# Optimization experiments

Hardware: AMD Instinct MI355X
Metric: run time of the kernel (lower is better)

## Reference

```python
import jax, jax.numpy as jnp
import numpy as np

N = 10000      # num nodes
E = 320000     # num edges
IN = 256       # in_dim
MP = 256       # mp_width
FL = 512       # fl_width
OUT = 64       # out_dim


def setup_inputs() -> dict:
    key = jax.random.key(0)
    ks = jax.random.split(key, 20)
    inp = {}
    inp["x"] = jax.random.normal(ks[0], (N, IN), dtype=jnp.float32)
    inp["edge_index"] = jax.random.randint(ks[1], (2, E), 0, N, dtype=jnp.int64)
    # iMP (frozen) linear layers: weight ~ N(0, 1) per nn.init.normal_(std=1.0)
    inp["mp_w0"] = jax.random.normal(ks[2], (IN, MP), dtype=jnp.float32)
    inp["mp_b0"] = jax.random.uniform(ks[3], (MP,), minval=-1.0, maxval=1.0) / np.sqrt(IN)
    inp["mp_w1"] = jax.random.normal(ks[4], (MP, MP), dtype=jnp.float32)
    inp["mp_b1"] = jax.random.uniform(ks[5], (MP,), minval=-1.0, maxval=1.0) / np.sqrt(MP)
    inp["mp_w2"] = jax.random.normal(ks[6], (MP, MP), dtype=jnp.float32)
    inp["mp_b2"] = jax.random.uniform(ks[7], (MP,), minval=-1.0, maxval=1.0) / np.sqrt(MP)
    # FC layers (torch default Linear init scale ~ 1/sqrt(fan_in))
    inp["fc_w0"] = jax.random.normal(ks[8], (MP, FL), dtype=jnp.float32) / np.sqrt(MP)
    inp["fc_b0"] = jnp.zeros((FL,), dtype=jnp.float32)
    inp["fc_w1"] = jax.random.normal(ks[9], (FL, FL), dtype=jnp.float32) / np.sqrt(FL)
    inp["fc_b1"] = jnp.zeros((FL,), dtype=jnp.float32)
    # injection projections
    inp["inj_w0"] = jax.random.normal(ks[10], (MP, FL), dtype=jnp.float32) / np.sqrt(MP)
    inp["inj_b0"] = jnp.zeros((FL,), dtype=jnp.float32)
    inp["inj_w1"] = jax.random.normal(ks[11], (MP, FL), dtype=jnp.float32) / np.sqrt(MP)
    inp["inj_b1"] = jnp.zeros((FL,), dtype=jnp.float32)
    inp["alpha"] = jnp.array(1.0, dtype=jnp.float32)
    inp["out_w"] = jax.random.normal(ks[12], (FL, OUT), dtype=jnp.float32) / np.sqrt(FL)
    inp["out_b"] = jnp.zeros((OUT,), dtype=jnp.float32)
    return inp


def _imp(x, w, b, row, col, deg_inv):
    # h = relu(W x); h /= deg; Ah = scatter_add over row of h[col]
    h = jax.nn.relu(x @ w + b) * deg_inv[:, None]      # [N, out]
    return jnp.zeros_like(h).at[row].add(h[col])       # gather + scatter-add


def reference(x, edge_index, mp_w0, mp_b0, mp_w1, mp_b1, mp_w2, mp_b2,
              fc_w0, fc_b0, fc_w1, fc_b1, inj_w0, inj_b0, inj_w1, inj_b1,
              alpha, out_w, out_b):
    row, col = edge_index[0], edge_index[1]
    deg = jax.ops.segment_sum(jnp.ones((E,), x.dtype), col, num_segments=N)
    # nodes with deg==0 never appear in col so clamping does not change output
    deg_inv = 1.0 / jnp.maximum(deg, 1.0)

    h = _imp(x, mp_w0, mp_b0, row, col, deg_inv)
    h = _imp(h, mp_w1, mp_b1, row, col, deg_inv)
    h = _imp(h, mp_w2, mp_b2, row, col, deg_inv)

    x_inject = h
    h = alpha * (jax.nn.relu(h) @ fc_w0 + fc_b0) + (x_inject @ inj_w0 + inj_b0)
    h = alpha * (jax.nn.relu(h) @ fc_w1 + fc_b1) + (x_inject @ inj_w1 + inj_b1)
    return h @ out_w + out_b
```

## Files before the change

### kernel.cpp

```cpp
#include <hip/hip_runtime.h>

#define N_NODES 10000
#define N_EDGES 320000
#define MPAD 10112
#define NBIN 10048
#define CAP 128
#define EBLKS 157
#define PREP_BLOCKS 512
#define PREP_TOT 1148480L

typedef unsigned short u16;
typedef short bf16x8 __attribute__((ext_vector_type(8)));
typedef float f32x4 __attribute__((ext_vector_type(4)));

__device__ __forceinline__ u16 f2b(float f) {
  unsigned u = __builtin_bit_cast(unsigned, f);
  unsigned r = u + 0x7fffu + ((u >> 16) & 1u);
  return (u16)(r >> 16);
}
__device__ __forceinline__ unsigned pack2(float a, float b) {
  return (unsigned)f2b(a) | ((unsigned)f2b(b) << 16);
}
__device__ __forceinline__ float blo(unsigned u) { return __builtin_bit_cast(float, u << 16); }
__device__ __forceinline__ float bhi(unsigned u) { return __builtin_bit_cast(float, u & 0xffff0000u); }

struct PP {
  const float *x; const int *ei;
  const float *w0, *w1, *w2, *fcw0, *injw0, *fcw1, *injw1, *outw;
  const float *fcb0, *injb0, *fcb1, *injb1, *alpha, *outb;
  u16 *xb, *w0t, *w1t, *w2t, *wc1t, *wft;
  float *bias1, *bf;
  int *cursor, *deg; u16 *csr;
};

__global__ __launch_bounds__(256) void prep_place(PP P) {
  const int tid = threadIdx.x, bid = blockIdx.x;

  if (bid < EBLKS) {
    const int e0 = bid * 2048;
#pragma unroll
    for (int j = 0; j < 2048; j += 256) {
      int e = e0 + j + tid;
      if (e < N_EDGES) {
        int r = P.ei[e];
        int c = P.ei[N_EDGES + e];
        int pos = atomicAdd(&P.cursor[r], 1);
        if (pos < CAP) P.csr[r * CAP + pos] = (u16)c;
        atomicAdd(&P.deg[c], 1);
      }
    }
    return;
  }

  const float alpha = P.alpha[0];
  const long stride = (long)PREP_BLOCKS * 256;
  for (long ii = (long)(bid - EBLKS) * 256 + tid; ii < PREP_TOT; ii += stride) {
    long i = ii;
    if (i < 640000L) {
      float4 v = ((const float4*)P.x)[i];
      uint2 o;
      o.x = pack2(v.x, v.y);
      o.y = pack2(v.z, v.w);
      *(uint2*)(P.xb + 4 * i) = o;
      continue;
    }
    i -= 640000L;
    if (i < 65536) { P.w0t[i] = f2b(P.w0[(i & 255) * 256 + (i >> 8)]); continue; }
    i -= 65536;
    if (i < 65536) { P.w1t[i] = f2b(P.w1[(i & 255) * 256 + (i >> 8)]); continue; }
    i -= 65536;
    if (i < 65536) { P.w2t[i] = f2b(P.w2[(i & 255) * 256 + (i >> 8)]); continue; }
    i -= 65536;
    if (i < 262144) {
      int n = (int)(i >> 9), k = (int)(i & 511);
      float v = (k < 256) ? alpha * P.fcw0[k * 512 + n] : P.injw0[(k - 256) * 512 + n];
      P.wc1t[i] = f2b(v); continue;
    }
    i -= 262144;
    if (i < 49152) {
      int n = (int)(i & 63), k = (int)(i >> 6);
      const float* fr = (k < 512) ? P.fcw1 + (size_t)k * 512
                                  : P.injw1 + (size_t)(k - 512) * 512;
      float a0 = 0.f, a1 = 0.f, a2 = 0.f, a3 = 0.f;
#pragma unroll 4
      for (int j = 0; j < 512; j += 4) {
        float4 f = *(const float4*)(fr + j);
        a0 += f.x * P.outw[(j + 0) * 64 + n];
        a1 += f.y * P.outw[(j + 1) * 64 + n];
        a2 += f.z * P.outw[(j + 2) * 64 + n];
        a3 += f.w * P.outw[(j + 3) * 64 + n];
      }
      float acc = (a0 + a1) + (a2 + a3);
      if (k < 512) acc *= alpha;
      P.wft[n * 768 + k] = f2b(acc);
      continue;
    }
    i -= 49152;
    if (i < 64) {
      float acc = P.outb[i];
#pragma unroll 8
      for (int j = 0; j < 512; ++j)
        acc += (alpha * P.fcb1[j] + P.injb1[j]) * P.outw[j * 64 + i];
      P.bf[i] = acc;
      continue;
    }
    i -= 64;
    if (i < 512) { P.bias1[i] = alpha * P.fcb0[i] + P.injb0[i]; continue; }
  }
}

template<int K, bool RELU, bool SCALE, bool F32OUT>
__global__ __launch_bounds__(128) void gemm64(
    const u16* __restrict__ A, int lda,
    const u16* __restrict__ Bt,
    const float* __restrict__ bias,
    const int* __restrict__ deg,
    u16* __restrict__ Cb, float* __restrict__ Cf, int ldc)
{
  __shared__ u16 As[64 * 72];
  __shared__ u16 Bs[64 * 72];
  const int tid = threadIdx.x;
  const int m0 = blockIdx.x * 64;
  const int n0 = blockIdx.y * 64;
  const int wave = tid >> 6;
  const int lane = tid & 63;
  const int wr = wave * 32;
  const int lm = lane & 15;
  const int koff = (lane >> 4) * 8;

  const int srow = tid >> 2;
  const int scol = (tid & 3) * 16;
  const u16* Ag0 = A + (size_t)(m0 + srow) * lda + scol;
  const u16* Ag1 = A + (size_t)(m0 + srow + 32) * lda + scol;
  const u16* Bg0 = Bt + (size_t)(n0 + srow) * K + scol;
  const u16* Bg1 = Bt + (size_t)(n0 + srow + 32) * K + scol;
  u16* Asw0 = &As[srow * 72 + scol];
  u16* Asw1 = &As[(srow + 32) * 72 + scol];
  u16* Bsw0 = &Bs[srow * 72 + scol];
  u16* Bsw1 = &Bs[(srow + 32) * 72 + scol];

  f32x4 acc[2][4] = {};

  int4 pa0 = *(const int4*)(Ag0),     pa1 = *(const int4*)(Ag0 + 8);
  int4 pa2 = *(const int4*)(Ag1),     pa3 = *(const int4*)(Ag1 + 8);
  int4 pb0 = *(const int4*)(Bg0),     pb1 = *(const int4*)(Bg0 + 8);
  int4 pb2 = *(const int4*)(Bg1),     pb3 = *(const int4*)(Bg1 + 8);

#pragma unroll
  for (int kb = 0; kb < K; kb += 64) {
    __syncthreads();
    *(int4*)Asw0 = pa0; *(int4*)(Asw0 + 8) = pa1;
    *(int4*)Asw1 = pa2; *(int4*)(Asw1 + 8) = pa3;
    *(int4*)Bsw0 = pb0; *(int4*)(Bsw0 + 8) = pb1;
    *(int4*)Bsw1 = pb2; *(int4*)(Bsw1 + 8) = pb3;
    __syncthreads();
    if (kb + 64 < K) {
      pa0 = *(const int4*)(Ag0 + kb + 64); pa1 = *(const int4*)(Ag0 + kb + 72);
      pa2 = *(const int4*)(Ag1 + kb + 64); pa3 = *(const int4*)(Ag1 + kb + 72);
      pb0 = *(const int4*)(Bg0 + kb + 64); pb1 = *(const int4*)(Bg0 + kb + 72);
      pb2 = *(const int4*)(Bg1 + kb + 64); pb3 = *(const int4*)(Bg1 + kb + 72);
    }
#pragma unroll
    for (int ks = 0; ks < 2; ++ks) {
      bf16x8 af[2], bf[4];
#pragma unroll
      for (int mi = 0; mi < 2; ++mi)
        af[mi] = *(const bf16x8*)&As[(wr + mi * 16 + lm) * 72 + ks * 32 + koff];
#pragma unroll
      for (int ni = 0; ni < 4; ++ni)
        bf[ni] = *(const bf16x8*)&Bs[(ni * 16 + lm) * 72 + ks * 32 + koff];
#pragma unroll
      for (int mi = 0; mi < 2; ++mi)
#pragma unroll
        for (int ni = 0; ni < 4; ++ni)
          acc[mi][ni] = __builtin_amdgcn_mfma_f32_16x16x32_bf16(af[mi], bf[ni], acc[mi][ni], 0, 0, 0);
    }
  }

  const int q4 = (lane >> 4) * 4;
#pragma unroll
  for (int mi = 0; mi < 2; ++mi) {
#pragma unroll
    for (int ni = 0; ni < 4; ++ni) {
      const int gc = n0 + ni * 16 + lm;
      const float bv = bias[gc];
#pragma unroll
      for (int r = 0; r < 4; ++r) {
        const int gr = m0 + wr + mi * 16 + q4 + r;
        float v = acc[mi][ni][r] + bv;
        if (RELU) v = fmaxf(v, 0.f);
        if (SCALE) v *= 1.0f / fmaxf((float)deg[gr], 1.0f);
        if (F32OUT) {
          if (gr < N_NODES) Cf[(size_t)gr * ldc + gc] = v;
        } else {
          Cb[(size_t)gr * ldc + gc] = f2b(v);
        }
      }
    }
  }
}

__global__ __launch_bounds__(256) void gemm_fc1(
    const u16* __restrict__ A,
    const u16* __restrict__ Bt,
    const float* __restrict__ bias,
    u16* __restrict__ Cb)
{
  const int K = 512;
  __shared__ u16 As[64 * 72];
  __shared__ u16 Bs[128 * 72];
  const int tid = threadIdx.x;
  const int m0 = blockIdx.x * 64;
  const int n0 = blockIdx.y * 128;
  const int wave = tid >> 6;
  const int lane = tid & 63;
  const int wr = (wave >> 1) * 32;
  const int wc = (wave & 1) * 64;
  const int lm = lane & 15;
  const int koff = (lane >> 4) * 8;

  const int srow = tid >> 2;
  const int scol = (tid & 3) * 16;
  const u16* Ag  = A  + (size_t)(m0 + srow) * 512 + scol;
  const u16* Bg0 = Bt + (size_t)(n0 + srow) * K + scol;
  const u16* Bg1 = Bt + (size_t)(n0 + srow + 64) * K + scol;
  u16* Asw  = &As[srow * 72 + scol];
  u16* Bsw0 = &Bs[srow * 72 + scol];
  u16* Bsw1 = &Bs[(srow + 64) * 72 + scol];

  f32x4 acc[2][4] = {};

  int4 pa0 = *(const int4*)(Ag),      pa1 = *(const int4*)(Ag + 8);
  int4 pb0 = *(const int4*)(Bg0),     pb1 = *(const int4*)(Bg0 + 8);
  int4 pb2 = *(const int4*)(Bg1),     pb3 = *(const int4*)(Bg1 + 8);

#pragma unroll
  for (int kb = 0; kb < K; kb += 64) {
    __syncthreads();
    *(int4*)Asw = pa0;  *(int4*)(Asw + 8) = pa1;
    *(int4*)Bsw0 = pb0; *(int4*)(Bsw0 + 8) = pb1;
    *(int4*)Bsw1 = pb2; *(int4*)(Bsw1 + 8) = pb3;
    __syncthreads();
    if (kb + 64 < K) {
      pa0 = *(const int4*)(Ag + kb + 64);  pa1 = *(const int4*)(Ag + kb + 72);
      pb0 = *(const int4*)(Bg0 + kb + 64); pb1 = *(const int4*)(Bg0 + kb + 72);
      pb2 = *(const int4*)(Bg1 + kb + 64); pb3 = *(const int4*)(Bg1 + kb + 72);
    }
#pragma unroll
    for (int ks = 0; ks < 2; ++ks) {
      bf16x8 af[2], bf[4];
#pragma unroll
      for (int mi = 0; mi < 2; ++mi)
        af[mi] = *(const bf16x8*)&As[(wr + mi * 16 + lm) * 72 + ks * 32 + koff];
#pragma unroll
      for (int ni = 0; ni < 4; ++ni)
        bf[ni] = *(const bf16x8*)&Bs[(wc + ni * 16 + lm) * 72 + ks * 32 + koff];
#pragma unroll
      for (int mi = 0; mi < 2; ++mi)
#pragma unroll
        for (int ni = 0; ni < 4; ++ni)
          acc[mi][ni] = __builtin_amdgcn_mfma_f32_16x16x32_bf16(af[mi], bf[ni], acc[mi][ni], 0, 0, 0);
    }
  }

  const int q4 = (lane >> 4) * 4;
#pragma unroll
  for (int mi = 0; mi < 2; ++mi) {
#pragma unroll
    for (int ni = 0; ni < 4; ++ni) {
      const int gc = n0 + wc + ni * 16 + lm;
      const float bv = bias[gc];
#pragma unroll
      for (int r = 0; r < 4; ++r) {
        const int gr = m0 + wr + mi * 16 + q4 + r;
        Cb[(size_t)gr * 512 + gc] = f2b(fmaxf(acc[mi][ni][r] + bv, 0.f));
      }
    }
  }
}

__global__ __launch_bounds__(128) void gemm_fold(
    const u16* __restrict__ Ar,
    const u16* __restrict__ Ah,
    const u16* __restrict__ Bt,
    const float* __restrict__ bias,
    float* __restrict__ Cf)
{
  const int K = 768;
  __shared__ u16 As[64 * 72];
  __shared__ u16 Bs[64 * 72];
  const int tid = threadIdx.x;
  const int m0 = blockIdx.x * 64;
  const int n0 = 0;
  const int wave = tid >> 6;
  const int lane = tid & 63;
  const int wr = wave * 32;
  const int lm = lane & 15;
  const int koff = (lane >> 4) * 8;

  const int srow = tid >> 2;
  const int scol = (tid & 3) * 16;
  const int ar0 = m0 + srow, ar1 = m0 + srow + 32;
  auto aptr = [&](int row, int col) -> const u16* {
    return (col < 512) ? Ar + (size_t)row * 512 + col
                       : Ah + (size_t)row * 512 + (col - 512);
  };
  const u16* Bg0 = Bt + (size_t)(n0 + srow) * K + scol;
  const u16* Bg1 = Bt + (size_t)(n0 + srow + 32) * K + scol;
  u16* Asw0 = &As[srow * 72 + scol];
  u16* Asw1 = &As[(srow + 32) * 72 + scol];
  u16* Bsw0 = &Bs[srow * 72 + scol];
  u16* Bsw1 = &Bs[(srow + 32) * 72 + scol];

  f32x4 acc[2][4] = {};

  int4 pa0 = *(const int4*)aptr(ar0, scol);
  int4 pa1 = *(const int4*)aptr(ar0, scol + 8);
  int4 pa2 = *(const int4*)aptr(ar1, scol);
  int4 pa3 = *(const int4*)aptr(ar1, scol + 8);
  int4 pb0 = *(const int4*)(Bg0), pb1 = *(const int4*)(Bg0 + 8);
  int4 pb2 = *(const int4*)(Bg1), pb3 = *(const int4*)(Bg1 + 8);

#pragma unroll
  for (int kb = 0; kb < K; kb += 64) {
    __syncthreads();
    *(int4*)Asw0 = pa0; *(int4*)(Asw0 + 8) = pa1;
    *(int4*)Asw1 = pa2; *(int4*)(Asw1 + 8) = pa3;
    *(int4*)Bsw0 = pb0; *(int4*)(Bsw0 + 8) = pb1;
    *(int4*)Bsw1 = pb2; *(int4*)(Bsw1 + 8) = pb3;
    __syncthreads();
    if (kb + 64 < K) {
      int c = kb + 64 + scol;
      pa0 = *(const int4*)aptr(ar0, c);
      pa1 = *(const int4*)aptr(ar0, c + 8);
      pa2 = *(const int4*)aptr(ar1, c);
      pa3 = *(const int4*)aptr(ar1, c + 8);
      pb0 = *(const int4*)(Bg0 + kb + 64); pb1 = *(const int4*)(Bg0 + kb + 72);
      pb2 = *(const int4*)(Bg1 + kb + 64); pb3 = *(const int4*)(Bg1 + kb + 72);
    }
#pragma unroll
    for (int ks = 0; ks < 2; ++ks) {
      bf16x8 af[2], bf[4];
#pragma unroll
      for (int mi = 0; mi < 2; ++mi)
        af[mi] = *(const bf16x8*)&As[(wr + mi * 16 + lm) * 72 + ks * 32 + koff];
#pragma unroll
      for (int ni = 0; ni < 4; ++ni)
        bf[ni] = *(const bf16x8*)&Bs[(ni * 16 + lm) * 72 + ks * 32 + koff];
#pragma unroll
      for (int mi = 0; mi < 2; ++mi)
#pragma unroll
        for (int ni = 0; ni < 4; ++ni)
          acc[mi][ni] = __builtin_amdgcn_mfma_f32_16x16x32_bf16(af[mi], bf[ni], acc[mi][ni], 0, 0, 0);
    }
  }

  const int q4 = (lane >> 4) * 4;
#pragma unroll
  for (int mi = 0; mi < 2; ++mi) {
#pragma unroll
    for (int ni = 0; ni < 4; ++ni) {
      const int gc = ni * 16 + lm;
      const float bv = bias[gc];
#pragma unroll
      for (int r = 0; r < 4; ++r) {
        const int gr = m0 + wr + mi * 16 + q4 + r;
        if (gr < N_NODES) Cf[(size_t)gr * 64 + gc] = acc[mi][ni][r] + bv;
      }
    }
  }
}

__global__ __launch_bounds__(256) void aggregate(
    const u16* __restrict__ tmp, const int* __restrict__ cnt,
    const u16* __restrict__ csr, u16* __restrict__ out0,
    u16* __restrict__ A1, int mode)
{
  const int wv = threadIdx.x >> 6;
  const int lane = threadIdx.x & 63;
  const int r = blockIdx.x * 4 + wv;
  const int half = lane >> 5;
  const int q = lane & 31;
  int n = cnt[r]; if (n > CAP) n = CAP;
  const int beg = r * CAP, end = beg + n;
  const size_t feat = (size_t)q * 16;
  const char* tb = (const char*)tmp;

  float s0 = 0.f, s1 = 0.f, s2 = 0.f, s3 = 0.f, s4 = 0.f, s5 = 0.f, s6 = 0.f, s7 = 0.f;
  int i = beg;
  for (; i + 16 <= end; i += 16) {
    uint4 v[8];
#pragma unroll
    for (int j = 0; j < 8; ++j)
      v[j] = *(const uint4*)(tb + (size_t)csr[i + 2 * j + half] * 512 + feat);
#pragma unroll
    for (int j = 0; j < 8; ++j) {
      s0 += blo(v[j].x); s1 += bhi(v[j].x); s2 += blo(v[j].y); s3 += bhi(v[j].y);
      s4 += blo(v[j].z); s5 += bhi(v[j].z); s6 += blo(v[j].w); s7 += bhi(v[j].w);
    }
  }
  for (; i + 8 <= end; i += 8) {
    uint4 v[4];
#pragma unroll
    for (int j = 0; j < 4; ++j)
      v[j] = *(const uint4*)(tb + (size_t)csr[i + 2 * j + half] * 512 + feat);
#pragma unroll
    for (int j = 0; j < 4; ++j) {
      s0 += blo(v[j].x); s1 += bhi(v[j].x); s2 += blo(v[j].y); s3 += bhi(v[j].y);
      s4 += blo(v[j].z); s5 += bhi(v[j].z); s6 += blo(v[j].w); s7 += bhi(v[j].w);
    }
  }
  for (; i < end; i += 2) {
    int id = i + half;
    if (id < end) {
      uint4 v = *(const uint4*)(tb + (size_t)csr[id] * 512 + feat);
      s0 += blo(v.x); s1 += bhi(v.x); s2 += blo(v.y); s3 += bhi(v.y);
      s4 += blo(v.z); s5 += bhi(v.z); s6 += blo(v.w); s7 += bhi(v.w);
    }
  }
  const int src = lane ^ 32;
  s0 += __shfl(s0, src, 64); s1 += __shfl(s1, src, 64);
  s2 += __shfl(s2, src, 64); s3 += __shfl(s3, src, 64);
  s4 += __shfl(s4, src, 64); s5 += __shfl(s5, src, 64);
  s6 += __shfl(s6, src, 64); s7 += __shfl(s7, src, 64);

  if (half == 0) {
    uint4 pv;
    pv.x = pack2(s0, s1); pv.y = pack2(s2, s3);
    pv.z = pack2(s4, s5); pv.w = pack2(s6, s7);
    if (mode == 0) {
      *(uint4*)((char*)out0 + (size_t)r * 512 + feat) = pv;
    } else {
      uint4 pr;
      pr.x = pack2(fmaxf(s0, 0.f), fmaxf(s1, 0.f));
      pr.y = pack2(fmaxf(s2, 0.f), fmaxf(s3, 0.f));
      pr.z = pack2(fmaxf(s4, 0.f), fmaxf(s5, 0.f));
      pr.w = pack2(fmaxf(s6, 0.f), fmaxf(s7, 0.f));
      *(uint4*)((char*)A1 + (size_t)r * 1024 + feat) = pr;
      *(uint4*)((char*)A1 + (size_t)r * 1024 + 512 + feat) = pv;
    }
  }
}

extern "C" void kernel_launch(void* const* d_in, const int* in_sizes, int n_in,
                              void* d_out, int out_size, void* d_ws, size_t ws_size,
                              hipStream_t stream) {
  const int* ei = (const int*)d_in[1];

  char* p = (char*)d_ws;
  auto carve = [&](size_t bytes) -> void* {
    void* r = (void*)p;
    p += (bytes + 255) & ~(size_t)255;
    return r;
  };
  int*   deg     = (int*)carve(MPAD * 4);
  int*   cursor  = (int*)carve(NBIN * 4);
  u16*   csr     = (u16*)carve((size_t)NBIN * CAP * 2);
  float* bias1   = (float*)carve(512 * 4);
  float* bf      = (float*)carve(64 * 4);
  u16* xb    = (u16*)carve((size_t)MPAD * 256 * 2);
  u16* w0t   = (u16*)carve(65536 * 2);
  u16* w1t   = (u16*)carve(65536 * 2);
  u16* w2t   = (u16*)carve(65536 * 2);
  u16* wc1t  = (u16*)carve(262144 * 2);
  u16* wft   = (u16*)carve(49152 * 2);
  u16* tmp   = (u16*)carve((size_t)MPAD * 256 * 2);
  u16* h     = (u16*)carve((size_t)MPAD * 256 * 2);
  u16* cat1  = (u16*)carve((size_t)MPAD * 512 * 2);
  u16* relu1 = (u16*)carve((size_t)MPAD * 512 * 2);

  PP pp;
  pp.x = (const float*)d_in[0];
  pp.ei = ei;
  pp.w0 = (const float*)d_in[2];
  pp.w1 = (const float*)d_in[4];
  pp.w2 = (const float*)d_in[6];
  pp.fcw0 = (const float*)d_in[8];
  pp.fcw1 = (const float*)d_in[10];
  pp.injw0 = (const float*)d_in[12];
  pp.injw1 = (const float*)d_in[14];
  pp.outw = (const float*)d_in[17];
  pp.fcb0 = (const float*)d_in[9];
  pp.injb0 = (const float*)d_in[13];
  pp.fcb1 = (const float*)d_in[11];
  pp.injb1 = (const float*)d_in[15];
  pp.alpha = (const float*)d_in[16];
  pp.outb = (const float*)d_in[18];
  pp.xb = xb; pp.w0t = w0t; pp.w1t = w1t; pp.w2t = w2t;
  pp.wc1t = wc1t; pp.wft = wft;
  pp.bias1 = bias1; pp.bf = bf;
  pp.cursor = cursor; pp.deg = deg; pp.csr = csr;

  const float* mp_b0 = (const float*)d_in[3];
  const float* mp_b1 = (const float*)d_in[5];
  const float* mp_b2 = (const float*)d_in[7];
  float* out = (float*)d_out;

  hipMemsetAsync(deg, 0, (size_t)(MPAD + NBIN) * 4, stream);
  prep_place<<<EBLKS + PREP_BLOCKS, 256, 0, stream>>>(pp);

  dim3 gmp(MPAD / 64, 4), gfc(MPAD / 64, 4), go(MPAD / 64, 1);
  gemm64<256, true, true, false><<<gmp, 128, 0, stream>>>(xb, 256, w0t, mp_b0, deg, tmp, nullptr, 256);
  aggregate<<<2500, 256, 0, stream>>>(tmp, cursor, csr, h, nullptr, 0);
  gemm64<256, true, true, false><<<gmp, 128, 0, stream>>>(h, 256, w1t, mp_b1, deg, tmp, nullptr, 256);
  aggregate<<<2500, 256, 0, stream>>>(tmp, cursor, csr, h, nullptr, 0);
  gemm64<256, true, true, false><<<gmp, 128, 0, stream>>>(h, 256, w2t, mp_b2, deg, tmp, nullptr, 256);
  aggregate<<<2500, 256, 0, stream>>>(tmp, cursor, csr, nullptr, cat1, 1);
  gemm_fc1<<<gfc, 256, 0, stream>>>(cat1, wc1t, bias1, relu1);
  gemm_fold<<<go, 128, 0, stream>>>(relu1, cat1 + 256, wft, bf, out);
}
```

Measured before the change: 233.3 us.

## Use 4-wave blocks in MP GEMM and swap grid axes for A-tile reuse

The message-passing GEMM now uses 256-thread blocks with four waves, each owning 16 rows of the 64x64 tile instead of two waves owning 32 rows each. This halves the per-thread accumulators and global loads and raises waves per block. The grid axes are swapped in both the MP GEMM and the fc1 GEMM so that consecutive blocks share the same A row tile, which should improve L2 reuse of the activations. The unused F32OUT path is removed. Each wave now does less MFMA work per LDS read of B, so LDS traffic per flop goes up.

Measured after the change: 229.7 us. No clear change (-1.5%).

```diff
diff --git a/kernel.cpp b/kernel.cpp
--- a/kernel.cpp
+++ b/kernel.cpp
@@ -109,93 +109,72 @@
   }
 }
 
-template<int K, bool RELU, bool SCALE, bool F32OUT>
-__global__ __launch_bounds__(128) void gemm64(
+template<int K, bool RELU, bool SCALE>
+__global__ __launch_bounds__(256) void gemm64(
     const u16* __restrict__ A, int lda,
     const u16* __restrict__ Bt,
     const float* __restrict__ bias,
     const int* __restrict__ deg,
-    u16* __restrict__ Cb, float* __restrict__ Cf, int ldc)
+    u16* __restrict__ Cb, int ldc)
 {
   __shared__ u16 As[64 * 72];
   __shared__ u16 Bs[64 * 72];
   const int tid = threadIdx.x;
-  const int m0 = blockIdx.x * 64;
-  const int n0 = blockIdx.y * 64;
+  const int m0 = blockIdx.y * 64;
+  const int n0 = blockIdx.x * 64;
   const int wave = tid >> 6;
   const int lane = tid & 63;
-  const int wr = wave * 32;
+  const int wr = wave * 16;
   const int lm = lane & 15;
   const int koff = (lane >> 4) * 8;
 
   const int srow = tid >> 2;
   const int scol = (tid & 3) * 16;
-  const u16* Ag0 = A + (size_t)(m0 + srow) * lda + scol;
-  const u16* Ag1 = A + (size_t)(m0 + srow + 32) * lda + scol;
-  const u16* Bg0 = Bt + (size_t)(n0 + srow) * K + scol;
-  const u16* Bg1 = Bt + (size_t)(n0 + srow + 32) * K + scol;
-  u16* Asw0 = &As[srow * 72 + scol];
-  u16* Asw1 = &As[(srow + 32) * 72 + scol];
-  u16* Bsw0 = &Bs[srow * 72 + scol];
-  u16* Bsw1 = &Bs[(srow + 32) * 72 + scol];
-
-  f32x4 acc[2][4] = {};
-
-  int4 pa0 = *(const int4*)(Ag0),     pa1 = *(const int4*)(Ag0 + 8);
-  int4 pa2 = *(const int4*)(Ag1),     pa3 = *(const int4*)(Ag1 + 8);
-  int4 pb0 = *(const int4*)(Bg0),     pb1 = *(const int4*)(Bg0 + 8);
-  int4 pb2 = *(const int4*)(Bg1),     pb3 = *(const int4*)(Bg1 + 8);
+  const u16* Ag = A + (size_t)(m0 + srow) * lda + scol;
+  const u16* Bg = Bt + (size_t)(n0 + srow) * K + scol;
+  u16* Asw = &As[srow * 72 + scol];
+  u16* Bsw = &Bs[srow * 72 + scol];
+
+  f32x4 acc[4] = {};
+
+  int4 pa0 = *(const int4*)(Ag), pa1 = *(const int4*)(Ag + 8);
+  int4 pb0 = *(const int4*)(Bg), pb1 = *(const int4*)(Bg + 8);
 
 #pragma unroll
   for (int kb = 0; kb < K; kb += 64) {
     __syncthreads();
-    *(int4*)Asw0 = pa0; *(int4*)(Asw0 + 8) = pa1;
-    *(int4*)Asw1 = pa2; *(int4*)(Asw1 + 8) = pa3;
-    *(int4*)Bsw0 = pb0; *(int4*)(Bsw0 + 8) = pb1;
-    *(int4*)Bsw1 = pb2; *(int4*)(Bsw1 + 8) = pb3;
+    *(int4*)Asw = pa0; *(int4*)(Asw + 8) = pa1;
+    *(int4*)Bsw = pb0; *(int4*)(Bsw + 8) = pb1;
     __syncthreads();
     if (kb + 64 < K) {
-      pa0 = *(const int4*)(Ag0 + kb + 64); pa1 = *(const int4*)(Ag0 + kb + 72);
-      pa2 = *(const int4*)(Ag1 + kb + 64); pa3 = *(const int4*)(Ag1 + kb + 72);
-      pb0 = *(const int4*)(Bg0 + kb + 64); pb1 = *(const int4*)(Bg0 + kb + 72);
-      pb2 = *(const int4*)(Bg1 + kb + 64); pb3 = *(const int4*)(Bg1 + kb + 72);
+      pa0 = *(const int4*)(Ag + kb + 64); pa1 = *(const int4*)(Ag + kb + 72);
+      pb0 = *(const int4*)(Bg + kb + 64); pb1 = *(const int4*)(Bg + kb + 72);
     }
 #pragma unroll
     for (int ks = 0; ks < 2; ++ks) {
-      bf16x8 af[2], bf[4];
-#pragma unroll
-      for (int mi = 0; mi < 2; ++mi)
-        af[mi] = *(const bf16x8*)&As[(wr + mi * 16 + lm) * 72 + ks * 32 + koff];
+      bf16x8 af, bf[4];
+      af = *(const bf16x8*)&As[(wr + lm) * 72 + ks * 32 + koff];
 #pragma unroll
       for (int ni = 0; ni < 4; ++ni)
         bf[ni] = *(const bf16x8*)&Bs[(ni * 16 + lm) * 72 + ks * 32 + koff];
 #pragma unroll
-      for (int mi = 0; mi < 2; ++mi)
-#pragma unroll
-        for (int ni = 0; ni < 4; ++ni)
-          acc[mi][ni] = __builtin_amdgcn_mfma_f32_16x16x32_bf16(af[mi], bf[ni], acc[mi][ni], 0, 0, 0);
+      for (int ni = 0; ni < 4; ++ni)
+        acc[ni] = __builtin_amdgcn_mfma_f32_16x16x32_bf16(af, bf[ni], acc[ni], 0, 0, 0);
     }
   }
 
   const int q4 = (lane >> 4) * 4;
 #pragma unroll
-  for (int mi = 0; mi < 2; ++mi) {
-#pragma unroll
-    for (int ni = 0; ni < 4; ++ni) {
-      const int gc = n0 + ni * 16 + lm;
-      const float bv = bias[gc];
-#pragma unroll
-      for (int r = 0; r < 4; ++r) {
-        const int gr = m0 + wr + mi * 16 + q4 + r;
-        float v = acc[mi][ni][r] + bv;
-        if (RELU) v = fmaxf(v, 0.f);
-        if (SCALE) v *= 1.0f / fmaxf((float)deg[gr], 1.0f);
-        if (F32OUT) {
-          if (gr < N_NODES) Cf[(size_t)gr * ldc + gc] = v;
-        } else {
-          Cb[(size_t)gr * ldc + gc] = f2b(v);
-        }
-      }
+  for (int ni = 0; ni < 4; ++ni) {
+    const int gc = n0 + ni * 16 + lm;
+    const float bv = bias[gc];
+#pragma unroll
+    for (int r = 0; r < 4; ++r) {
+      const int gr = m0 + wr + q4 + r;
+      float v = acc[ni][r] + bv;
+      if (RELU) v = fmaxf(v, 0.f);
+      if (SCALE) v *= 1.0f / fmaxf((float)deg[gr], 1.0f);
+      Cb[(size_t)gr * ldc + gc] = f2b(v);
     }
   }
 }
@@ -210,8 +189,8 @@
   __shared__ u16 As[64 * 72];
   __shared__ u16 Bs[128 * 72];
   const int tid = threadIdx.x;
-  const int m0 = blockIdx.x * 64;
-  const int n0 = blockIdx.y * 128;
+  const int m0 = blockIdx.y * 64;
+  const int n0 = blockIdx.x * 128;
   const int wave = tid >> 6;
   const int lane = tid & 63;
   const int wr = (wave >> 1) * 32;
@@ -499,12 +478,12 @@
   hipMemsetAsync(deg, 0, (size_t)(MPAD + NBIN) * 4, stream);
   prep_place<<<EBLKS + PREP_BLOCKS, 256, 0, stream>>>(pp);
 
-  dim3 gmp(MPAD / 64, 4), gfc(MPAD / 64, 4), go(MPAD / 64, 1);
-  gemm64<256, true, true, false><<<gmp, 128, 0, stream>>>(xb, 256, w0t, mp_b0, deg, tmp, nullptr, 256);
+  dim3 gmp(4, MPAD / 64), gfc(4, MPAD / 64), go(MPAD / 64, 1);
+  gemm64<256, true, true><<<gmp, 256, 0, stream>>>(xb, 256, w0t, mp_b0, deg, tmp, 256);
   aggregate<<<2500, 256, 0, stream>>>(tmp, cursor, csr, h, nullptr, 0);
-  gemm64<256, true, true, false><<<gmp, 128, 0, stream>>>(h, 256, w1t, mp_b1, deg, tmp, nullptr, 256);
+  gemm64<256, true, true><<<gmp, 256, 0, stream>>>(h, 256, w1t, mp_b1, deg, tmp, 256);
   aggregate<<<2500, 256, 0, stream>>>(tmp, cursor, csr, h, nullptr, 0);
-  gemm64<256, true, true, false><<<gmp, 128, 0, stream>>>(h, 256, w2t, mp_b2, deg, tmp, nullptr, 256);
+  gemm64<256, true, true><<<gmp, 256, 0, stream>>>(h, 256, w2t, mp_b2, deg, tmp, 256);
   aggregate<<<2500, 256, 0, stream>>>(tmp, cursor, csr, nullptr, cat1, 1);
   gemm_fc1<<<gfc, 256, 0, stream>>>(cat1, wc1t, bias1, relu1);
   gemm_fold<<<go, 128, 0, stream>>>(relu1, cat1 + 256, wft, bf, out);
```
